# Kernel tuning notes

Measured on AMD Instinct MI355X. Metric: run time of the kernel, lower is better.

Reference implementation:

```python
import jax, jax.numpy as jnp
import numpy as np

N, E, G, L, D = 50000, 800000, 512, 3, 128
BN_EPS = 1e-5


def setup_inputs() -> dict:
    key = jax.random.key(0)
    ks = jax.random.split(key, 16)
    x = jax.random.normal(ks[0], (N, D), dtype=jnp.float32)
    edge_index = jax.random.randint(ks[1], (2, E), 0, N)
    batch = jnp.sort(jax.random.randint(ks[2], (N,), 0, G))
    W1 = jax.random.normal(ks[3], (L, D, D), dtype=jnp.float32) * 0.05
    b1 = jax.random.normal(ks[4], (L, D), dtype=jnp.float32) * 0.05
    gamma = jax.random.uniform(ks[5], (L, D), dtype=jnp.float32) + 0.5
    beta = jax.random.normal(ks[6], (L, D), dtype=jnp.float32) * 0.05
    running_mean = jax.random.normal(ks[7], (L, D), dtype=jnp.float32) * 0.1
    running_var = jax.random.uniform(ks[8], (L, D), dtype=jnp.float32) + 0.5
    W2 = jax.random.normal(ks[9], (L, D, D), dtype=jnp.float32) * 0.05
    b2 = jax.random.normal(ks[10], (L, D), dtype=jnp.float32) * 0.05
    lin1_W = jax.random.normal(ks[11], (L * D, L * D), dtype=jnp.float32) * 0.05
    lin1_b = jax.random.normal(ks[12], (L * D,), dtype=jnp.float32) * 0.05
    lin2_W = jax.random.normal(ks[13], (L * D, 10), dtype=jnp.float32) * 0.05
    lin2_b = jax.random.normal(ks[14], (10,), dtype=jnp.float32) * 0.05
    return {"x": x, "edge_index": edge_index, "batch": batch,
            "W1": W1, "b1": b1, "gamma": gamma, "beta": beta,
            "running_mean": running_mean, "running_var": running_var,
            "W2": W2, "b2": b2, "lin1_W": lin1_W, "lin1_b": lin1_b,
            "lin2_W": lin2_W, "lin2_b": lin2_b}


def _gin_layer(h, src, dst, W1, b1, gamma, beta, rm, rv, W2, b2):
    # GINConv (eps=0): MLP((1+eps)*x + sum_{j->i} x_j); aggregate src->dst
    agg = jax.ops.segment_sum(h[src], dst, num_segments=N)  # [N, D]
    z = (h + agg) @ W1 + b1
    # BatchNorm1d in eval mode (running stats)
    z = (z - rm) * (gamma / jnp.sqrt(rv + BN_EPS)) + beta
    z = jax.nn.relu(z)
    return jax.nn.relu(z @ W2 + b2)


def reference(x, edge_index, batch, W1, b1, gamma, beta, running_mean,
              running_var, W2, b2, lin1_W, lin1_b, lin2_W, lin2_b):
    src, dst = edge_index[0], edge_index[1]
    h = x
    pooled = []
    for i in range(L):
        h = _gin_layer(h, src, dst, W1[i], b1[i], gamma[i], beta[i],
                       running_mean[i], running_var[i], W2[i], b2[i])
        pooled.append(jax.ops.segment_sum(h, batch, num_segments=G))  # [G, D]
    g = jnp.concatenate(pooled, axis=1)  # [G, L*D]
    g = jax.nn.relu(g @ lin1_W + lin1_b)
    # dropout is identity in eval mode
    return g @ lin2_W + lin2_b  # [G, num_classes]
```

## Files before the change

### kernel.cpp

```cpp
#include <hip/hip_runtime.h>
#include <hip/hip_bf16.h>

#define D_FEAT 128
#define N_GRAPHS 512
#define N_LAYERS 3
#define POOL_DIM (N_LAYERS * D_FEAT)
#define N_CLASSES 10
#define BN_EPS 1e-5f
#define CAP 64

typedef __attribute__((ext_vector_type(8))) short bf16x8;
typedef __attribute__((ext_vector_type(8))) unsigned short ushort8;
typedef __attribute__((ext_vector_type(4))) float f32x4;

__device__ __forceinline__ unsigned short f2bf(float f) {
    unsigned u = __builtin_bit_cast(unsigned, f);
    u += 0x7FFFu + ((u >> 16) & 1u);
    return (unsigned short)(u >> 16);
}
__device__ __forceinline__ float bf2f(unsigned short h) {
    unsigned u = ((unsigned)h) << 16;
    return __builtin_bit_cast(float, u);
}
__device__ __forceinline__ float bf_lo(unsigned u) {
    return __builtin_bit_cast(float, u << 16);
}
__device__ __forceinline__ float bf_hi(unsigned u) {
    return __builtin_bit_cast(float, u & 0xffff0000u);
}

__global__ __launch_bounds__(256) void fill_v2(const int* __restrict__ ei,
                                               int* __restrict__ cursor,
                                               int* __restrict__ bucket, int E, int N) {
    int r = blockIdx.x & 7;
    int chunk = blockIdx.x >> 3;
    int nchunks = gridDim.x >> 3;
    int per = (E + nchunks - 1) / nchunks;
    int e0 = chunk * per;
    int e1 = e0 + per; if (e1 > E) e1 = E;
    int span = (N + 7) >> 3;
    int lo = r * span;
    int hi = lo + span; if (hi > N) hi = N;
    for (int e = e0 + threadIdx.x; e < e1; e += 256) {
        int dst = ei[E + e];
        if (dst >= lo && dst < hi) {
            int src = ei[e];
            int pos = atomicAdd(&cursor[dst], 1);
            if (pos < CAP) bucket[(size_t)dst * CAP + pos] = src;
        }
    }
}

__global__ void prep_kernel(const float* __restrict__ b1, const float* __restrict__ gamma,
                            const float* __restrict__ beta, const float* __restrict__ rm,
                            const float* __restrict__ rv, const float* __restrict__ b2,
                            float* __restrict__ ea, float* __restrict__ eb) {
    int i = blockIdx.x * 256 + threadIdx.x;
    if (i >= N_LAYERS * D_FEAT) return;
    int l = i >> 7, c = i & 127;
    float s = gamma[i] * rsqrtf(rv[i] + BN_EPS);
    ea[(2 * l) * D_FEAT + c] = s;
    eb[(2 * l) * D_FEAT + c] = (b1[i] - rm[i]) * s + beta[i];
    ea[(2 * l + 1) * D_FEAT + c] = 1.0f;
    eb[(2 * l + 1) * D_FEAT + c] = b2[i];
}

__global__ void cvt_x(const float* __restrict__ x, unsigned short* __restrict__ xb, int n4) {
    int i = blockIdx.x * 256 + threadIdx.x;
    if (i < n4) {
        float4 v = ((const float4*)x)[i];
        ushort4 o;
        o.x = f2bf(v.x); o.y = f2bf(v.y); o.z = f2bf(v.z); o.w = f2bf(v.w);
        ((ushort4*)xb)[i] = o;
    }
}

__global__ void cvt_w(const float* __restrict__ W1, const float* __restrict__ W2,
                      unsigned short* __restrict__ Wt) {
    int idx = blockIdx.x * 256 + threadIdx.x;
    if (idx >= 2 * N_LAYERS * D_FEAT * D_FEAT) return;
    int slot = idx >> 14;
    int r = (idx >> 7) & 127;
    int c = idx & 127;
    int l = slot >> 1;
    const float* W = (slot & 1) ? W2 : W1;
    Wt[idx] = f2bf(W[(size_t)l * D_FEAT * D_FEAT + (size_t)c * D_FEAT + r]);
}

__global__ __launch_bounds__(256) void agg_kernel(const unsigned short* __restrict__ hprev,
                                                  const int* __restrict__ deg,
                                                  const int* __restrict__ bucket,
                                                  unsigned short* __restrict__ y, int n) {
    int wave = threadIdx.x >> 6, lane = threadIdx.x & 63;
    int n0 = (blockIdx.x * 4 + wave) * 2;
    if (n0 >= n) return;
    int n1 = n0 + 1;
    bool v1 = (n1 < n);
    int d0 = deg[n0]; if (d0 > CAP) d0 = CAP;
    int d1 = v1 ? deg[n1] : 0; if (d1 > CAP) d1 = CAP;
    int grp = lane >> 4, sub = lane & 15;
    const uint4* hp = (const uint4*)hprev;

    int idx0 = bucket[(size_t)n0 * CAP + lane];
    int idx1 = v1 ? bucket[(size_t)n1 * CAP + lane] : 0;

    float a0[8] = {0.f,0.f,0.f,0.f,0.f,0.f,0.f,0.f};
    float a1[8] = {0.f,0.f,0.f,0.f,0.f,0.f,0.f,0.f};
    int dmax = d0 > d1 ? d0 : d1;

    for (int t = 0; t < dmax; t += 16) {
        bool p0[4], p1[4];
        int r0[4], r1[4];
        #pragma unroll
        for (int q = 0; q < 4; ++q) {
            int e = t + q * 4 + grp;
            int s0 = __shfl(idx0, e & 63);
            int s1 = __shfl(idx1, e & 63);
            p0[q] = e < d0;
            p1[q] = e < d1;
            r0[q] = p0[q] ? s0 : n0;
            r1[q] = p1[q] ? s1 : n0;
        }
        uint4 w0[4], w1[4];
        #pragma unroll
        for (int q = 0; q < 4; ++q) {
            w0[q] = hp[(size_t)r0[q] * 16 + sub];
            w1[q] = hp[(size_t)r1[q] * 16 + sub];
        }
        #pragma unroll
        for (int q = 0; q < 4; ++q) {
            if (p0[q]) {
                uint4 v = w0[q];
                a0[0] += bf_lo(v.x); a0[1] += bf_hi(v.x);
                a0[2] += bf_lo(v.y); a0[3] += bf_hi(v.y);
                a0[4] += bf_lo(v.z); a0[5] += bf_hi(v.z);
                a0[6] += bf_lo(v.w); a0[7] += bf_hi(v.w);
            }
            if (p1[q]) {
                uint4 v = w1[q];
                a1[0] += bf_lo(v.x); a1[1] += bf_hi(v.x);
                a1[2] += bf_lo(v.y); a1[3] += bf_hi(v.y);
                a1[4] += bf_lo(v.z); a1[5] += bf_hi(v.z);
                a1[6] += bf_lo(v.w); a1[7] += bf_hi(v.w);
            }
        }
    }

    #pragma unroll
    for (int j = 0; j < 8; ++j) {
        a0[j] += __shfl_xor(a0[j], 16);
        a0[j] += __shfl_xor(a0[j], 32);
        a1[j] += __shfl_xor(a1[j], 16);
        a1[j] += __shfl_xor(a1[j], 32);
    }

    uint4 s0v = hp[(size_t)n0 * 16 + sub];
    a0[0] += bf_lo(s0v.x); a0[1] += bf_hi(s0v.x);
    a0[2] += bf_lo(s0v.y); a0[3] += bf_hi(s0v.y);
    a0[4] += bf_lo(s0v.z); a0[5] += bf_hi(s0v.z);
    a0[6] += bf_lo(s0v.w); a0[7] += bf_hi(s0v.w);
    if (v1) {
        uint4 s1v = hp[(size_t)n1 * 16 + sub];
        a1[0] += bf_lo(s1v.x); a1[1] += bf_hi(s1v.x);
        a1[2] += bf_lo(s1v.y); a1[3] += bf_hi(s1v.y);
        a1[4] += bf_lo(s1v.z); a1[5] += bf_hi(s1v.z);
        a1[6] += bf_lo(s1v.w); a1[7] += bf_hi(s1v.w);
    }

    if (grp == 0) {
        uint4 o;
        o.x = (unsigned)f2bf(a0[0]) | ((unsigned)f2bf(a0[1]) << 16);
        o.y = (unsigned)f2bf(a0[2]) | ((unsigned)f2bf(a0[3]) << 16);
        o.z = (unsigned)f2bf(a0[4]) | ((unsigned)f2bf(a0[5]) << 16);
        o.w = (unsigned)f2bf(a0[6]) | ((unsigned)f2bf(a0[7]) << 16);
        ((uint4*)y)[(size_t)n0 * 16 + sub] = o;
        if (v1) {
            uint4 p;
            p.x = (unsigned)f2bf(a1[0]) | ((unsigned)f2bf(a1[1]) << 16);
            p.y = (unsigned)f2bf(a1[2]) | ((unsigned)f2bf(a1[3]) << 16);
            p.z = (unsigned)f2bf(a1[4]) | ((unsigned)f2bf(a1[5]) << 16);
            p.w = (unsigned)f2bf(a1[6]) | ((unsigned)f2bf(a1[7]) << 16);
            ((uint4*)y)[(size_t)n1 * 16 + sub] = p;
        }
    }
}

__global__ __launch_bounds__(256) void layer_fused(const unsigned short* __restrict__ A,
                                                   const unsigned short* __restrict__ Wt1,
                                                   const unsigned short* __restrict__ Wt2,
                                                   const float* __restrict__ ea1,
                                                   const float* __restrict__ eb1,
                                                   const float* __restrict__ ea2,
                                                   const float* __restrict__ eb2,
                                                   const int* __restrict__ batch,
                                                   float* __restrict__ pooled, int loff,
                                                   unsigned short* __restrict__ outh, int n) {
    __shared__ unsigned short As[64][136];
    __shared__ unsigned short Ws[128][136];
    __shared__ int bgsh[64];
    int tid = threadIdx.x;
    int row0 = blockIdx.x * 64;
    int wave = tid >> 6, lane = tid & 63;
    int m0 = wave * 16;
    int lrow = lane & 15, lq = lane >> 4;

    #pragma unroll
    for (int i = 0; i < 4; ++i) {
        int idx = tid + i * 256;
        int r = idx >> 4, c = (idx & 15) * 8;
        ushort8 v = (ushort8)0;
        if (row0 + r < n) v = *(const ushort8*)&A[(size_t)(row0 + r) * D_FEAT + c];
        *(ushort8*)&As[r][c] = v;
    }
    #pragma unroll
    for (int i = 0; i < 8; ++i) {
        int idx = tid + i * 256;
        int r = idx >> 4, c = (idx & 15) * 8;
        *(ushort8*)&Ws[r][c] = *(const ushort8*)&Wt1[(size_t)r * D_FEAT + c];
    }
    if (tid < 64)
        bgsh[tid] = (row0 + tid < n) ? batch[row0 + tid] : -1;
    __syncthreads();

    f32x4 acc[8] = {};
    #pragma unroll
    for (int t = 0; t < 4; ++t) {
        bf16x8 a = *(const bf16x8*)&As[m0 + lrow][t * 32 + lq * 8];
        #pragma unroll
        for (int nt = 0; nt < 8; ++nt) {
            bf16x8 b = *(const bf16x8*)&Ws[nt * 16 + lrow][t * 32 + lq * 8];
            acc[nt] = __builtin_amdgcn_mfma_f32_16x16x32_bf16(a, b, acc[nt], 0, 0, 0);
        }
    }
    __syncthreads();

    #pragma unroll
    for (int nt = 0; nt < 8; ++nt) {
        int col = nt * 16 + lrow;
        float al = ea1[col], be = eb1[col];
        #pragma unroll
        for (int r = 0; r < 4; ++r) {
            float v = fmaxf(fmaf(acc[nt][r], al, be), 0.f);
            As[m0 + lq * 4 + r][col] = f2bf(v);
        }
    }
    #pragma unroll
    for (int i = 0; i < 8; ++i) {
        int idx = tid + i * 256;
        int r = idx >> 4, c = (idx & 15) * 8;
        *(ushort8*)&Ws[r][c] = *(const ushort8*)&Wt2[(size_t)r * D_FEAT + c];
    }
    __syncthreads();

    f32x4 acc2[8] = {};
    #pragma unroll
    for (int t = 0; t < 4; ++t) {
        bf16x8 a = *(const bf16x8*)&As[m0 + lrow][t * 32 + lq * 8];
        #pragma unroll
        for (int nt = 0; nt < 8; ++nt) {
            bf16x8 b = *(const bf16x8*)&Ws[nt * 16 + lrow][t * 32 + lq * 8];
            acc2[nt] = __builtin_amdgcn_mfma_f32_16x16x32_bf16(a, b, acc2[nt], 0, 0, 0);
        }
    }

    #pragma unroll
    for (int nt = 0; nt < 8; ++nt) {
        int col = nt * 16 + lrow;
        float al = ea2[col], be = eb2[col];
        #pragma unroll
        for (int r = 0; r < 4; ++r) {
            int grow = row0 + m0 + lq * 4 + r;
            if (grow < n) {
                float v = fmaxf(fmaf(acc2[nt][r], al, be), 0.f);
                outh[(size_t)grow * D_FEAT + col] = f2bf(v);
            }
        }
    }

    __syncthreads();
    float* Wsf = (float*)Ws;
    #pragma unroll
    for (int nt = 0; nt < 8; ++nt) {
        int col = nt * 16 + lrow;
        float al = ea2[col], be = eb2[col];
        #pragma unroll
        for (int r = 0; r < 4; ++r) {
            int lr = m0 + lq * 4 + r;
            float v = fmaxf(fmaf(acc2[nt][r], al, be), 0.f);
            Wsf[lr * 132 + col] = bf2f(f2bf(v));
        }
    }
    __syncthreads();

    int c = tid & 127, half = tid >> 7;
    int rbeg = half * 32, rend = rbeg + 32;
    int cur = -1; float sum = 0.f;
    for (int r = rbeg; r < rend; ++r) {
        int g = bgsh[r];
        if (g != cur) {
            if (cur >= 0) atomicAdd(&pooled[(size_t)cur * POOL_DIM + loff + c], sum);
            cur = g; sum = 0.f;
        }
        if (g >= 0) sum += Wsf[r * 132 + c];
    }
    if (cur >= 0) atomicAdd(&pooled[(size_t)cur * POOL_DIM + loff + c], sum);
}

__global__ void fc1_kernel(const float* __restrict__ pooled, const float* __restrict__ W,
                           const float* __restrict__ b, float* __restrict__ out) {
    int idx = blockIdx.x * 256 + threadIdx.x;
    if (idx >= N_GRAPHS * POOL_DIM) return;
    int r = idx / POOL_DIM, c = idx % POOL_DIM;
    float s = b[c];
    const float* prow = pooled + (size_t)r * POOL_DIM;
    for (int k = 0; k < POOL_DIM; ++k)
        s = fmaf(prow[k], W[(size_t)k * POOL_DIM + c], s);
    out[idx] = fmaxf(s, 0.f);
}

__global__ void fc2_kernel(const float* __restrict__ fc1o, const float* __restrict__ W,
                           const float* __restrict__ b, float* __restrict__ out) {
    int idx = blockIdx.x * 256 + threadIdx.x;
    if (idx >= N_GRAPHS * N_CLASSES) return;
    int r = idx / N_CLASSES, c = idx % N_CLASSES;
    float s = b[c];
    const float* prow = fc1o + (size_t)r * POOL_DIM;
    for (int k = 0; k < POOL_DIM; ++k)
        s = fmaf(prow[k], W[(size_t)k * N_CLASSES + c], s);
    out[idx] = s;
}

extern "C" void kernel_launch(void* const* d_in, const int* in_sizes, int n_in,
                              void* d_out, int out_size, void* d_ws, size_t ws_size,
                              hipStream_t stream) {
    const float* x      = (const float*)d_in[0];
    const int*   ei     = (const int*)  d_in[1];
    const int*   batch  = (const int*)  d_in[2];
    const float* W1     = (const float*)d_in[3];
    const float* b1     = (const float*)d_in[4];
    const float* gamma  = (const float*)d_in[5];
    const float* beta   = (const float*)d_in[6];
    const float* rm     = (const float*)d_in[7];
    const float* rv     = (const float*)d_in[8];
    const float* W2     = (const float*)d_in[9];
    const float* b2     = (const float*)d_in[10];
    const float* lin1W  = (const float*)d_in[11];
    const float* lin1b  = (const float*)d_in[12];
    const float* lin2W  = (const float*)d_in[13];
    const float* lin2b  = (const float*)d_in[14];
    float* out = (float*)d_out;

    const int N = in_sizes[0] / D_FEAT;
    const int E = in_sizes[1] / 2;

    char* ws = (char*)d_ws;
    auto carve = [&](size_t bytes) {
        char* p = ws;
        ws += (bytes + 255) & ~(size_t)255;
        return p;
    };
    int*   cursor    = (int*)  carve((size_t)N * 4);
    int*   bucket    = (int*)  carve((size_t)N * CAP * 4);
    float* ea        = (float*)carve((size_t)2 * N_LAYERS * D_FEAT * 4);
    float* eb        = (float*)carve((size_t)2 * N_LAYERS * D_FEAT * 4);
    unsigned short* Wt   = (unsigned short*)carve((size_t)2 * N_LAYERS * D_FEAT * D_FEAT * 2);
    unsigned short* xb   = (unsigned short*)carve((size_t)N * D_FEAT * 2);
    unsigned short* ybuf = (unsigned short*)carve((size_t)N * D_FEAT * 2);
    unsigned short* hbuf = (unsigned short*)carve((size_t)N * D_FEAT * 2);
    float* pooled    = (float*)carve((size_t)N_GRAPHS * POOL_DIM * 4);
    float* fc1o      = (float*)carve((size_t)N_GRAPHS * POOL_DIM * 4);

    hipMemsetAsync(cursor, 0, (size_t)N * 4, stream);
    hipMemsetAsync(pooled, 0, (size_t)N_GRAPHS * POOL_DIM * 4, stream);
    fill_v2<<<8 * 192, 256, 0, stream>>>(ei, cursor, bucket, E, N);
    prep_kernel<<<2, 256, 0, stream>>>(b1, gamma, beta, rm, rv, b2, ea, eb);
    cvt_x<<<(N * D_FEAT / 4 + 255) / 256, 256, 0, stream>>>(x, xb, N * D_FEAT / 4);
    cvt_w<<<(2 * N_LAYERS * D_FEAT * D_FEAT + 255) / 256, 256, 0, stream>>>(W1, W2, Wt);

    const unsigned short* hprev = xb;
    for (int l = 0; l < N_LAYERS; ++l) {
        agg_kernel<<<(N + 7) / 8, 256, 0, stream>>>(hprev, cursor, bucket, ybuf, N);
        layer_fused<<<(N + 63) / 64, 256, 0, stream>>>(ybuf,
                      Wt + (size_t)(2 * l) * D_FEAT * D_FEAT,
                      Wt + (size_t)(2 * l + 1) * D_FEAT * D_FEAT,
                      ea + (size_t)(2 * l) * D_FEAT,
                      eb + (size_t)(2 * l) * D_FEAT,
                      ea + (size_t)(2 * l + 1) * D_FEAT,
                      eb + (size_t)(2 * l + 1) * D_FEAT,
                      batch, pooled, l * D_FEAT, hbuf, N);
        hprev = hbuf;
    }
    fc1_kernel<<<(N_GRAPHS * POOL_DIM + 255) / 256, 256, 0, stream>>>(pooled, lin1W, lin1b, fc1o);
    fc2_kernel<<<(N_GRAPHS * N_CLASSES + 255) / 256, 256, 0, stream>>>(fc1o, lin2W, lin2b, out);
}
```

Measured before the change: 366.7 us.

## Fuse neighbor aggregation into layer GEMM kernel and bin edges before CSR fill

The separate aggregation kernel is removed. Its gather-sum now runs inside layer_fused, where each wave aggregates its 16 rows straight into shared memory before the MFMA GEMMs, so the intermediate aggregated buffer is never written to or read back from global memory. Edge bucketing becomes a two-pass scheme: edges are first partitioned into 8 destination bins, then a fill kernel handles each bin, so the edge list is no longer re-read 8 times. In exchange, the GEMM kernel now carries long-latency gathers that may lower occupancy and leave the MFMA units idle, and the binning adds a kernel and a pairs buffer.

Result: slower. 423.6 us (+15.5%).

```diff
diff --git a/kernel.cpp b/kernel.cpp
--- a/kernel.cpp
+++ b/kernel.cpp
@@ -8,6 +8,7 @@
 #define N_CLASSES 10
 #define BN_EPS 1e-5f
 #define CAP 64
+#define NBINS 8
 
 typedef __attribute__((ext_vector_type(8))) short bf16x8;
 typedef __attribute__((ext_vector_type(8))) unsigned short ushort8;
@@ -29,25 +30,48 @@
     return __builtin_bit_cast(float, u & 0xffff0000u);
 }
 
-__global__ __launch_bounds__(256) void fill_v2(const int* __restrict__ ei,
+__global__ __launch_bounds__(256) void bin_kernel(const int* __restrict__ ei, int E, int N,
+                                                  int2* __restrict__ pairs, int binCap,
+                                                  int* __restrict__ binCnt) {
+    __shared__ int hist[NBINS], base[NBINS], loc[NBINS];
+    int per = (E + gridDim.x - 1) / gridDim.x;
+    int e0 = blockIdx.x * per;
+    int e1 = e0 + per; if (e1 > E) e1 = E;
+    int span = (N + NBINS - 1) / NBINS;
+    if (threadIdx.x < NBINS) hist[threadIdx.x] = 0;
+    __syncthreads();
+    for (int e = e0 + threadIdx.x; e < e1; e += 256)
+        atomicAdd(&hist[ei[E + e] / span], 1);
+    __syncthreads();
+    if (threadIdx.x < NBINS) {
+        base[threadIdx.x] = atomicAdd(&binCnt[threadIdx.x], hist[threadIdx.x]);
+        loc[threadIdx.x] = 0;
+    }
+    __syncthreads();
+    for (int e = e0 + threadIdx.x; e < e1; e += 256) {
+        int dst = ei[E + e];
+        int src = ei[e];
+        int b = dst / span;
+        int p = base[b] + atomicAdd(&loc[b], 1);
+        pairs[(size_t)b * binCap + p] = make_int2(src, dst);
+    }
+}
+
+__global__ __launch_bounds__(256) void fill_v3(const int2* __restrict__ pairs,
+                                               const int* __restrict__ binCnt, int binCap,
                                                int* __restrict__ cursor,
-                                               int* __restrict__ bucket, int E, int N) {
+                                               int* __restrict__ bucket) {
     int r = blockIdx.x & 7;
     int chunk = blockIdx.x >> 3;
     int nchunks = gridDim.x >> 3;
-    int per = (E + nchunks - 1) / nchunks;
-    int e0 = chunk * per;
-    int e1 = e0 + per; if (e1 > E) e1 = E;
-    int span = (N + 7) >> 3;
-    int lo = r * span;
-    int hi = lo + span; if (hi > N) hi = N;
-    for (int e = e0 + threadIdx.x; e < e1; e += 256) {
-        int dst = ei[E + e];
-        if (dst >= lo && dst < hi) {
-            int src = ei[e];
-            int pos = atomicAdd(&cursor[dst], 1);
-            if (pos < CAP) bucket[(size_t)dst * CAP + pos] = src;
-        }
+    int cnt = binCnt[r];
+    int per = (cnt + nchunks - 1) / nchunks;
+    int p0 = chunk * per;
+    int p1 = p0 + per; if (p1 > cnt) p1 = cnt;
+    for (int p = p0 + threadIdx.x; p < p1; p += 256) {
+        int2 pr = pairs[(size_t)r * binCap + p];
+        int pos = atomicAdd(&cursor[pr.y], 1);
+        if (pos < CAP) bucket[(size_t)pr.y * CAP + pos] = pr.x;
     }
 }
 
@@ -87,105 +111,9 @@
     Wt[idx] = f2bf(W[(size_t)l * D_FEAT * D_FEAT + (size_t)c * D_FEAT + r]);
 }
 
-__global__ __launch_bounds__(256) void agg_kernel(const unsigned short* __restrict__ hprev,
-                                                  const int* __restrict__ deg,
-                                                  const int* __restrict__ bucket,
-                                                  unsigned short* __restrict__ y, int n) {
-    int wave = threadIdx.x >> 6, lane = threadIdx.x & 63;
-    int n0 = (blockIdx.x * 4 + wave) * 2;
-    if (n0 >= n) return;
-    int n1 = n0 + 1;
-    bool v1 = (n1 < n);
-    int d0 = deg[n0]; if (d0 > CAP) d0 = CAP;
-    int d1 = v1 ? deg[n1] : 0; if (d1 > CAP) d1 = CAP;
-    int grp = lane >> 4, sub = lane & 15;
-    const uint4* hp = (const uint4*)hprev;
-
-    int idx0 = bucket[(size_t)n0 * CAP + lane];
-    int idx1 = v1 ? bucket[(size_t)n1 * CAP + lane] : 0;
-
-    float a0[8] = {0.f,0.f,0.f,0.f,0.f,0.f,0.f,0.f};
-    float a1[8] = {0.f,0.f,0.f,0.f,0.f,0.f,0.f,0.f};
-    int dmax = d0 > d1 ? d0 : d1;
-
-    for (int t = 0; t < dmax; t += 16) {
-        bool p0[4], p1[4];
-        int r0[4], r1[4];
-        #pragma unroll
-        for (int q = 0; q < 4; ++q) {
-            int e = t + q * 4 + grp;
-            int s0 = __shfl(idx0, e & 63);
-            int s1 = __shfl(idx1, e & 63);
-            p0[q] = e < d0;
-            p1[q] = e < d1;
-            r0[q] = p0[q] ? s0 : n0;
-            r1[q] = p1[q] ? s1 : n0;
-        }
-        uint4 w0[4], w1[4];
-        #pragma unroll
-        for (int q = 0; q < 4; ++q) {
-            w0[q] = hp[(size_t)r0[q] * 16 + sub];
-            w1[q] = hp[(size_t)r1[q] * 16 + sub];
-        }
-        #pragma unroll
-        for (int q = 0; q < 4; ++q) {
-            if (p0[q]) {
-                uint4 v = w0[q];
-                a0[0] += bf_lo(v.x); a0[1] += bf_hi(v.x);
-                a0[2] += bf_lo(v.y); a0[3] += bf_hi(v.y);
-                a0[4] += bf_lo(v.z); a0[5] += bf_hi(v.z);
-                a0[6] += bf_lo(v.w); a0[7] += bf_hi(v.w);
-            }
-            if (p1[q]) {
-                uint4 v = w1[q];
-                a1[0] += bf_lo(v.x); a1[1] += bf_hi(v.x);
-                a1[2] += bf_lo(v.y); a1[3] += bf_hi(v.y);
-                a1[4] += bf_lo(v.z); a1[5] += bf_hi(v.z);
-                a1[6] += bf_lo(v.w); a1[7] += bf_hi(v.w);
-            }
-        }
-    }
-
-    #pragma unroll
-    for (int j = 0; j < 8; ++j) {
-        a0[j] += __shfl_xor(a0[j], 16);
-        a0[j] += __shfl_xor(a0[j], 32);
-        a1[j] += __shfl_xor(a1[j], 16);
-        a1[j] += __shfl_xor(a1[j], 32);
-    }
-
-    uint4 s0v = hp[(size_t)n0 * 16 + sub];
-    a0[0] += bf_lo(s0v.x); a0[1] += bf_hi(s0v.x);
-    a0[2] += bf_lo(s0v.y); a0[3] += bf_hi(s0v.y);
-    a0[4] += bf_lo(s0v.z); a0[5] += bf_hi(s0v.z);
-    a0[6] += bf_lo(s0v.w); a0[7] += bf_hi(s0v.w);
-    if (v1) {
-        uint4 s1v = hp[(size_t)n1 * 16 + sub];
-        a1[0] += bf_lo(s1v.x); a1[1] += bf_hi(s1v.x);
-        a1[2] += bf_lo(s1v.y); a1[3] += bf_hi(s1v.y);
-        a1[4] += bf_lo(s1v.z); a1[5] += bf_hi(s1v.z);
-        a1[6] += bf_lo(s1v.w); a1[7] += bf_hi(s1v.w);
-    }
-
-    if (grp == 0) {
-        uint4 o;
-        o.x = (unsigned)f2bf(a0[0]) | ((unsigned)f2bf(a0[1]) << 16);
-        o.y = (unsigned)f2bf(a0[2]) | ((unsigned)f2bf(a0[3]) << 16);
-        o.z = (unsigned)f2bf(a0[4]) | ((unsigned)f2bf(a0[5]) << 16);
-        o.w = (unsigned)f2bf(a0[6]) | ((unsigned)f2bf(a0[7]) << 16);
-        ((uint4*)y)[(size_t)n0 * 16 + sub] = o;
-        if (v1) {
-            uint4 p;
-            p.x = (unsigned)f2bf(a1[0]) | ((unsigned)f2bf(a1[1]) << 16);
-            p.y = (unsigned)f2bf(a1[2]) | ((unsigned)f2bf(a1[3]) << 16);
-            p.z = (unsigned)f2bf(a1[4]) | ((unsigned)f2bf(a1[5]) << 16);
-            p.w = (unsigned)f2bf(a1[6]) | ((unsigned)f2bf(a1[7]) << 16);
-            ((uint4*)y)[(size_t)n1 * 16 + sub] = p;
-        }
-    }
-}
-
-__global__ __launch_bounds__(256) void layer_fused(const unsigned short* __restrict__ A,
+__global__ __launch_bounds__(256) void layer_fused(const unsigned short* __restrict__ hprev,
+                                                   const int* __restrict__ deg,
+                                                   const int* __restrict__ bucket,
                                                    const unsigned short* __restrict__ Wt1,
                                                    const unsigned short* __restrict__ Wt2,
                                                    const float* __restrict__ ea1,
@@ -203,15 +131,9 @@
     int wave = tid >> 6, lane = tid & 63;
     int m0 = wave * 16;
     int lrow = lane & 15, lq = lane >> 4;
-
-    #pragma unroll
-    for (int i = 0; i < 4; ++i) {
-        int idx = tid + i * 256;
-        int r = idx >> 4, c = (idx & 15) * 8;
-        ushort8 v = (ushort8)0;
-        if (row0 + r < n) v = *(const ushort8*)&A[(size_t)(row0 + r) * D_FEAT + c];
-        *(ushort8*)&As[r][c] = v;
-    }
+    int grp = lane >> 4, sub = lane & 15;
+    const uint4* hp = (const uint4*)hprev;
+
     #pragma unroll
     for (int i = 0; i < 8; ++i) {
         int idx = tid + i * 256;
@@ -220,6 +142,99 @@
     }
     if (tid < 64)
         bgsh[tid] = (row0 + tid < n) ? batch[row0 + tid] : -1;
+
+    int nbase = row0 + m0;
+    for (int pass = 0; pass < 8; ++pass) {
+        int n0 = nbase + pass * 2;
+        int n1 = n0 + 1;
+        bool v0 = (n0 < n), v1 = (n1 < n);
+        int d0 = v0 ? deg[n0] : 0; if (d0 > CAP) d0 = CAP;
+        int d1 = v1 ? deg[n1] : 0; if (d1 > CAP) d1 = CAP;
+        int idx0 = v0 ? bucket[(size_t)n0 * CAP + lane] : 0;
+        int idx1 = v1 ? bucket[(size_t)n1 * CAP + lane] : 0;
+        int safe = v0 ? n0 : 0;
+
+        float a0[8] = {0.f,0.f,0.f,0.f,0.f,0.f,0.f,0.f};
+        float a1[8] = {0.f,0.f,0.f,0.f,0.f,0.f,0.f,0.f};
+        int dmax = d0 > d1 ? d0 : d1;
+
+        for (int t = 0; t < dmax; t += 16) {
+            bool p0[4], p1[4];
+            int r0[4], r1[4];
+            #pragma unroll
+            for (int q = 0; q < 4; ++q) {
+                int e = t + q * 4 + grp;
+                int s0 = __shfl(idx0, e & 63);
+                int s1 = __shfl(idx1, e & 63);
+                p0[q] = e < d0;
+                p1[q] = e < d1;
+                r0[q] = p0[q] ? s0 : safe;
+                r1[q] = p1[q] ? s1 : safe;
+            }
+            uint4 w0[4], w1[4];
+            #pragma unroll
+            for (int q = 0; q < 4; ++q) {
+                w0[q] = hp[(size_t)r0[q] * 16 + sub];
+                w1[q] = hp[(size_t)r1[q] * 16 + sub];
+            }
+            #pragma unroll
+            for (int q = 0; q < 4; ++q) {
+                if (p0[q]) {
+                    uint4 v = w0[q];
+                    a0[0] += bf_lo(v.x); a0[1] += bf_hi(v.x);
+                    a0[2] += bf_lo(v.y); a0[3] += bf_hi(v.y);
+                    a0[4] += bf_lo(v.z); a0[5] += bf_hi(v.z);
+                    a0[6] += bf_lo(v.w); a0[7] += bf_hi(v.w);
+                }
+                if (p1[q]) {
+                    uint4 v = w1[q];
+                    a1[0] += bf_lo(v.x); a1[1] += bf_hi(v.x);
+                    a1[2] += bf_lo(v.y); a1[3] += bf_hi(v.y);
+                    a1[4] += bf_lo(v.z); a1[5] += bf_hi(v.z);
+                    a1[6] += bf_lo(v.w); a1[7] += bf_hi(v.w);
+                }
+            }
+        }
+
+        #pragma unroll
+        for (int j = 0; j < 8; ++j) {
+            a0[j] += __shfl_xor(a0[j], 16);
+            a0[j] += __shfl_xor(a0[j], 32);
+            a1[j] += __shfl_xor(a1[j], 16);
+            a1[j] += __shfl_xor(a1[j], 32);
+        }
+
+        if (v0) {
+            uint4 sv = hp[(size_t)n0 * 16 + sub];
+            a0[0] += bf_lo(sv.x); a0[1] += bf_hi(sv.x);
+            a0[2] += bf_lo(sv.y); a0[3] += bf_hi(sv.y);
+            a0[4] += bf_lo(sv.z); a0[5] += bf_hi(sv.z);
+            a0[6] += bf_lo(sv.w); a0[7] += bf_hi(sv.w);
+        }
+        if (v1) {
+            uint4 sv = hp[(size_t)n1 * 16 + sub];
+            a1[0] += bf_lo(sv.x); a1[1] += bf_hi(sv.x);
+            a1[2] += bf_lo(sv.y); a1[3] += bf_hi(sv.y);
+            a1[4] += bf_lo(sv.z); a1[5] += bf_hi(sv.z);
+            a1[6] += bf_lo(sv.w); a1[7] += bf_hi(sv.w);
+        }
+
+        if (grp == 0) {
+            int lr = m0 + pass * 2;
+            uint4 o;
+            o.x = (unsigned)f2bf(a0[0]) | ((unsigned)f2bf(a0[1]) << 16);
+            o.y = (unsigned)f2bf(a0[2]) | ((unsigned)f2bf(a0[3]) << 16);
+            o.z = (unsigned)f2bf(a0[4]) | ((unsigned)f2bf(a0[5]) << 16);
+            o.w = (unsigned)f2bf(a0[6]) | ((unsigned)f2bf(a0[7]) << 16);
+            *(uint4*)&As[lr][sub * 8] = o;
+            uint4 p;
+            p.x = (unsigned)f2bf(a1[0]) | ((unsigned)f2bf(a1[1]) << 16);
+            p.y = (unsigned)f2bf(a1[2]) | ((unsigned)f2bf(a1[3]) << 16);
+            p.z = (unsigned)f2bf(a1[4]) | ((unsigned)f2bf(a1[5]) << 16);
+            p.w = (unsigned)f2bf(a1[6]) | ((unsigned)f2bf(a1[7]) << 16);
+            *(uint4*)&As[lr + 1][sub * 8] = p;
+        }
+    }
     __syncthreads();
 
     f32x4 acc[8] = {};
@@ -352,6 +367,7 @@
 
     const int N = in_sizes[0] / D_FEAT;
     const int E = in_sizes[1] / 2;
+    const int binCap = E / NBINS + 8192;
 
     char* ws = (char*)d_ws;
     auto carve = [&](size_t bytes) {
@@ -360,35 +376,40 @@
         return p;
     };
     int*   cursor    = (int*)  carve((size_t)N * 4);
+    int*   binCnt    = (int*)  carve((size_t)NBINS * 4);
     int*   bucket    = (int*)  carve((size_t)N * CAP * 4);
+    int2*  pairs     = (int2*) carve((size_t)NBINS * binCap * 8);
     float* ea        = (float*)carve((size_t)2 * N_LAYERS * D_FEAT * 4);
     float* eb        = (float*)carve((size_t)2 * N_LAYERS * D_FEAT * 4);
     unsigned short* Wt   = (unsigned short*)carve((size_t)2 * N_LAYERS * D_FEAT * D_FEAT * 2);
     unsigned short* xb   = (unsigned short*)carve((size_t)N * D_FEAT * 2);
-    unsigned short* ybuf = (unsigned short*)carve((size_t)N * D_FEAT * 2);
-    unsigned short* hbuf = (unsigned short*)carve((size_t)N * D_FEAT * 2);
+    unsigned short* hb0  = (unsigned short*)carve((size_t)N * D_FEAT * 2);
+    unsigned short* hb1  = (unsigned short*)carve((size_t)N * D_FEAT * 2);
     float* pooled    = (float*)carve((size_t)N_GRAPHS * POOL_DIM * 4);
     float* fc1o      = (float*)carve((size_t)N_GRAPHS * POOL_DIM * 4);
 
     hipMemsetAsync(cursor, 0, (size_t)N * 4, stream);
+    hipMemsetAsync(binCnt, 0, (size_t)NBINS * 4, stream);
     hipMemsetAsync(pooled, 0, (size_t)N_GRAPHS * POOL_DIM * 4, stream);
-    fill_v2<<<8 * 192, 256, 0, stream>>>(ei, cursor, bucket, E, N);
+    bin_kernel<<<256, 256, 0, stream>>>(ei, E, N, pairs, binCap, binCnt);
+    fill_v3<<<8 * 64, 256, 0, stream>>>(pairs, binCnt, binCap, cursor, bucket);
     prep_kernel<<<2, 256, 0, stream>>>(b1, gamma, beta, rm, rv, b2, ea, eb);
     cvt_x<<<(N * D_FEAT / 4 + 255) / 256, 256, 0, stream>>>(x, xb, N * D_FEAT / 4);
     cvt_w<<<(2 * N_LAYERS * D_FEAT * D_FEAT + 255) / 256, 256, 0, stream>>>(W1, W2, Wt);
 
     const unsigned short* hprev = xb;
+    unsigned short* hbufs[2] = { hb0, hb1 };
     for (int l = 0; l < N_LAYERS; ++l) {
-        agg_kernel<<<(N + 7) / 8, 256, 0, stream>>>(hprev, cursor, bucket, ybuf, N);
-        layer_fused<<<(N + 63) / 64, 256, 0, stream>>>(ybuf,
+        unsigned short* outh = hbufs[l & 1];
+        layer_fused<<<(N + 63) / 64, 256, 0, stream>>>(hprev, cursor, bucket,
                       Wt + (size_t)(2 * l) * D_FEAT * D_FEAT,
                       Wt + (size_t)(2 * l + 1) * D_FEAT * D_FEAT,
                       ea + (size_t)(2 * l) * D_FEAT,
                       eb + (size_t)(2 * l) * D_FEAT,
                       ea + (size_t)(2 * l + 1) * D_FEAT,
                       eb + (size_t)(2 * l + 1) * D_FEAT,
-                      batch, pooled, l * D_FEAT, hbuf, N);
-        hprev = hbuf;
+                      batch, pooled, l * D_FEAT, outh, N);
+        hprev = outh;
     }
     fc1_kernel<<<(N_GRAPHS * POOL_DIM + 255) / 256, 256, 0, stream>>>(pooled, lin1W, lin1b, fc1o);
     fc2_kernel<<<(N_GRAPHS * N_CLASSES + 255) / 256, 256, 0, stream>>>(fc1o, lin2W, lin2b, out);
```

## Pre-bin edges by destination range before bucket fill

Applied to the files above, without the earlier changes.

Replaces the single fill kernel, which had every block scan all edges and keep only those in its destination eighth, with two passes. The first pass partitions edges into 8 destination-range bins using shared-memory histograms and writes (src,dst) pairs. The second pass reads only its own bin's pairs and fills the per-node buckets. This stops each edge being read eight times, at the cost of an extra kernel launch and an intermediate pairs buffer. Each bin holds at most E/8 plus 8192 entries, so a skewed destination distribution could overflow it.

After: 378.0 us. 3.1% more time.

```diff
diff --git a/kernel.cpp b/kernel.cpp
--- a/kernel.cpp
+++ b/kernel.cpp
@@ -8,6 +8,8 @@
 #define N_CLASSES 10
 #define BN_EPS 1e-5f
 #define CAP 64
+#define NBINS 8
+
 
 typedef __attribute__((ext_vector_type(8))) short bf16x8;
 typedef __attribute__((ext_vector_type(8))) unsigned short ushort8;
@@ -29,25 +31,48 @@
     return __builtin_bit_cast(float, u & 0xffff0000u);
 }
 
-__global__ __launch_bounds__(256) void fill_v2(const int* __restrict__ ei,
+__global__ __launch_bounds__(256) void bin_kernel(const int* __restrict__ ei, int E, int N,
+                                                  int2* __restrict__ pairs, int binCap,
+                                                  int* __restrict__ binCnt) {
+    __shared__ int hist[NBINS], base[NBINS], loc[NBINS];
+    int per = (E + gridDim.x - 1) / gridDim.x;
+    int e0 = blockIdx.x * per;
+    int e1 = e0 + per; if (e1 > E) e1 = E;
+    int span = (N + NBINS - 1) / NBINS;
+    if (threadIdx.x < NBINS) hist[threadIdx.x] = 0;
+    __syncthreads();
+    for (int e = e0 + threadIdx.x; e < e1; e += 256)
+        atomicAdd(&hist[ei[E + e] / span], 1);
+    __syncthreads();
+    if (threadIdx.x < NBINS) {
+        base[threadIdx.x] = atomicAdd(&binCnt[threadIdx.x], hist[threadIdx.x]);
+        loc[threadIdx.x] = 0;
+    }
+    __syncthreads();
+    for (int e = e0 + threadIdx.x; e < e1; e += 256) {
+        int dst = ei[E + e];
+        int src = ei[e];
+        int b = dst / span;
+        int p = base[b] + atomicAdd(&loc[b], 1);
+        pairs[(size_t)b * binCap + p] = make_int2(src, dst);
+    }
+}
+
+__global__ __launch_bounds__(256) void fill_v3(const int2* __restrict__ pairs,
+                                               const int* __restrict__ binCnt, int binCap,
                                                int* __restrict__ cursor,
-                                               int* __restrict__ bucket, int E, int N) {
+                                               int* __restrict__ bucket) {
     int r = blockIdx.x & 7;
     int chunk = blockIdx.x >> 3;
     int nchunks = gridDim.x >> 3;
-    int per = (E + nchunks - 1) / nchunks;
-    int e0 = chunk * per;
-    int e1 = e0 + per; if (e1 > E) e1 = E;
-    int span = (N + 7) >> 3;
-    int lo = r * span;
-    int hi = lo + span; if (hi > N) hi = N;
-    for (int e = e0 + threadIdx.x; e < e1; e += 256) {
-        int dst = ei[E + e];
-        if (dst >= lo && dst < hi) {
-            int src = ei[e];
-            int pos = atomicAdd(&cursor[dst], 1);
-            if (pos < CAP) bucket[(size_t)dst * CAP + pos] = src;
-        }
+    int cnt = binCnt[r];
+    int per = (cnt + nchunks - 1) / nchunks;
+    int p0 = chunk * per;
+    int p1 = p0 + per; if (p1 > cnt) p1 = cnt;
+    for (int p = p0 + threadIdx.x; p < p1; p += 256) {
+        int2 pr = pairs[(size_t)r * binCap + p];
+        int pos = atomicAdd(&cursor[pr.y], 1);
+        if (pos < CAP) bucket[(size_t)pr.y * CAP + pos] = pr.x;
     }
 }
 
@@ -352,6 +377,7 @@
 
     const int N = in_sizes[0] / D_FEAT;
     const int E = in_sizes[1] / 2;
+    const int binCap = E / NBINS + 8192;
 
     char* ws = (char*)d_ws;
     auto carve = [&](size_t bytes) {
@@ -360,7 +386,9 @@
         return p;
     };
     int*   cursor    = (int*)  carve((size_t)N * 4);
+    int*   binCnt    = (int*)  carve((size_t)NBINS * 4);
     int*   bucket    = (int*)  carve((size_t)N * CAP * 4);
+    int2*  pairs     = (int2*) carve((size_t)NBINS * binCap * 8);
     float* ea        = (float*)carve((size_t)2 * N_LAYERS * D_FEAT * 4);
     float* eb        = (float*)carve((size_t)2 * N_LAYERS * D_FEAT * 4);
     unsigned short* Wt   = (unsigned short*)carve((size_t)2 * N_LAYERS * D_FEAT * D_FEAT * 2);
@@ -371,8 +399,10 @@
     float* fc1o      = (float*)carve((size_t)N_GRAPHS * POOL_DIM * 4);
 
     hipMemsetAsync(cursor, 0, (size_t)N * 4, stream);
+    hipMemsetAsync(binCnt, 0, (size_t)NBINS * 4, stream);
     hipMemsetAsync(pooled, 0, (size_t)N_GRAPHS * POOL_DIM * 4, stream);
-    fill_v2<<<8 * 192, 256, 0, stream>>>(ei, cursor, bucket, E, N);
+    bin_kernel<<<256, 256, 0, stream>>>(ei, E, N, pairs, binCap, binCnt);
+    fill_v3<<<8 * 64, 256, 0, stream>>>(pairs, binCnt, binCap, cursor, bucket);
     prep_kernel<<<2, 256, 0, stream>>>(b1, gamma, beta, rm, rv, b2, ea, eb);
     cvt_x<<<(N * D_FEAT / 4 + 255) / 256, 256, 0, stream>>>(x, xb, N * D_FEAT / 4);
     cvt_w<<<(2 * N_LAYERS * D_FEAT * D_FEAT + 255) / 256, 256, 0, stream>>>(W1, W2, Wt);
```
